# Kernel tuning notes

Hardware: AMD Instinct MI355X
Metric: run time of the kernel (lower is better)

## Reference

```python
import jax, jax.numpy as jnp
import numpy as np

N = 100_000   # nodes
E = 1_600_000 # edges (avg degree 16)
D = 64        # in_channel == out_channel (residual requires equality)
EPS = 1e-5    # BatchNorm1d eps


def setup_inputs() -> dict:
    key = jax.random.key(0)
    ks = jax.random.split(key, 8)
    x = jax.random.normal(ks[0], (N, D), dtype=jnp.float32)
    adj_val = jax.random.uniform(ks[1], (E,), dtype=jnp.float32) * 0.25  # sparse poly_adj values
    W = jax.random.normal(ks[2], (D, D), dtype=jnp.float32) / np.sqrt(D)  # Linear weight [out,in]
    b = jnp.zeros((D,), dtype=jnp.float32)
    gamma = jnp.ones((D,), dtype=jnp.float32)
    beta = jnp.zeros((D,), dtype=jnp.float32)
    adj_row = jax.random.randint(ks[3], (E,), 0, N, dtype=jnp.int32)
    adj_col = jax.random.randint(ks[4], (E,), 0, N, dtype=jnp.int32)
    return {"x": x, "adj_val": adj_val, "W": W, "b": b,
            "gamma": gamma, "beta": beta, "adj_row": adj_row, "adj_col": adj_col}


def reference(x, adj_val, W, b, gamma, beta, adj_row, adj_col):
    # h = poly_adj @ x  (COO SpMM via gather + segment_sum)
    h = jax.ops.segment_sum(adj_val[:, None] * x[adj_col], adj_row, num_segments=N)
    # Linear
    h = h @ W.T + b
    # residual
    h = h + x
    # BatchNorm1d (training-mode batch stats, biased variance)
    mean = jnp.mean(h, axis=0)
    var = jnp.mean(jnp.square(h - mean), axis=0)
    h = (h - mean) * jax.lax.rsqrt(var + EPS) * gamma + beta
    # ReLU (dropout with p=0 is identity)
    h = jax.nn.relu(h)
    return h
```

## Files before the change

### kernel.cpp

```cpp
#include <hip/hip_runtime.h>

#define DCH 64
#define BN_EPS 1e-5f

#define SUPSH 12
#define NSUPMAX 32
#define CAPS 67584
#define CHA 2048
#define CHB 2048
#define CPS 33
#define FPS 128
#define CAPF 704
#define CITER 8
#define SITER 3

__device__ __forceinline__ unsigned bf16pair(float lo, float hi) {
    unsigned ul = (__float_as_uint(lo) + 0x8000u) >> 16;
    unsigned uh = (__float_as_uint(hi) + 0x8000u) & 0xffff0000u;
    return ul | uh;
}
__device__ __forceinline__ float bf_lo(unsigned u) { return __uint_as_float(u << 16); }
__device__ __forceinline__ float bf_hi(unsigned u) { return __uint_as_float(u & 0xffff0000u); }

__global__ __launch_bounds__(256) void gemm_bin(const float* __restrict__ x,
                                                const float* __restrict__ W,
                                                unsigned short* __restrict__ yb,
                                                const int* __restrict__ rows,
                                                const int* __restrict__ cols,
                                                const float* __restrict__ vals,
                                                int* __restrict__ cursA,
                                                int2* __restrict__ edgesA,
                                                int N, int E, int GB, int BB,
                                                int NSUP) {
    __shared__ __align__(16) char smem[51200];
    const int tid = threadIdx.x;
    const int role = blockIdx.x & 1;
    const int idx = blockIdx.x >> 1;

    if (role == 0) {
        if (idx >= GB) return;
        float* xs = (float*)smem;
        float* wt = (float*)(smem + 34816);
        const int blockRow = idx * 128;

#pragma unroll
        for (int jj = 0; jj < 4; ++jj) {
            int idx4 = tid * 16 + jj * 4;
            int o = idx4 >> 6, k = idx4 & 63;
            float4 w4 = *(const float4*)&W[idx4];
            wt[(k + 0) * 64 + o] = w4.x;
            wt[(k + 1) * 64 + o] = w4.y;
            wt[(k + 2) * 64 + o] = w4.z;
            wt[(k + 3) * 64 + o] = w4.w;
        }
#pragma unroll
        for (int jj = 0; jj < 8; ++jj) {
            int f4 = tid + 256 * jj;
            int rl = f4 >> 4, k4 = (f4 & 15) * 4;
            int row = blockRow + rl;
            float4 v = make_float4(0.f, 0.f, 0.f, 0.f);
            if (row < N) v = *(const float4*)&x[row * DCH + k4];
            *(float4*)&xs[rl * 68 + k4] = v;
        }
        __syncthreads();

        const int tc = tid & 7;
        const int tr = tid >> 3;
        const int dc = tc * 8;
        float acc[4][8];
#pragma unroll
        for (int i = 0; i < 4; ++i)
#pragma unroll
            for (int j = 0; j < 8; ++j) acc[i][j] = 0.f;

        for (int k4 = 0; k4 < 16; ++k4) {
            float4 xv[4];
#pragma unroll
            for (int i = 0; i < 4; ++i)
                xv[i] = *(const float4*)&xs[(tr + 32 * i) * 68 + k4 * 4];
#pragma unroll
            for (int kk = 0; kk < 4; ++kk) {
                int k = k4 * 4 + kk;
                float4 w0 = *(const float4*)&wt[k * 64 + dc];
                float4 w1 = *(const float4*)&wt[k * 64 + dc + 4];
#pragma unroll
                for (int i = 0; i < 4; ++i) {
                    float xvi = (kk == 0) ? xv[i].x : (kk == 1) ? xv[i].y
                               : (kk == 2) ? xv[i].z : xv[i].w;
                    acc[i][0] = fmaf(xvi, w0.x, acc[i][0]);
                    acc[i][1] = fmaf(xvi, w0.y, acc[i][1]);
                    acc[i][2] = fmaf(xvi, w0.z, acc[i][2]);
                    acc[i][3] = fmaf(xvi, w0.w, acc[i][3]);
                    acc[i][4] = fmaf(xvi, w1.x, acc[i][4]);
                    acc[i][5] = fmaf(xvi, w1.y, acc[i][5]);
                    acc[i][6] = fmaf(xvi, w1.z, acc[i][6]);
                    acc[i][7] = fmaf(xvi, w1.w, acc[i][7]);
                }
            }
        }
#pragma unroll
        for (int i = 0; i < 4; ++i) {
            int row = blockRow + tr + 32 * i;
            if (row < N) {
                uint4 p;
                p.x = bf16pair(acc[i][0], acc[i][1]);
                p.y = bf16pair(acc[i][2], acc[i][3]);
                p.z = bf16pair(acc[i][4], acc[i][5]);
                p.w = bf16pair(acc[i][6], acc[i][7]);
                *(uint4*)&yb[row * DCH + dc] = p;
            }
        }
    } else {
        if (idx >= BB) return;
        int2* stage = (int2*)smem;
        unsigned char* bOf = (unsigned char*)(smem + 16384);
        int* hist   = (int*)(smem + 18432);
        int* startB = (int*)(smem + 18560);
        int* gbase  = (int*)(smem + 18688);
        const int lane = tid & 63, wave = tid >> 6;
        const int base = idx * CHA;
        const int cnt = min(CHA, E - base);

        for (int i = tid; i < NSUPMAX; i += 256) hist[i] = 0;
        __syncthreads();

        int myr[CITER], mycol[CITER], myrank[CITER];
        float myv[CITER];
#pragma unroll
        for (int it = 0; it < CITER; ++it) {
            int k = tid + it * 256;
            if (k < cnt) {
                int r = rows[base + k];
                myr[it] = r;
                mycol[it] = cols[base + k];
                myv[it] = vals[base + k];
                myrank[it] = atomicAdd(&hist[r >> SUPSH], 1);
            }
        }
        __syncthreads();
        if (wave == 0) {
            int v = (lane < NSUP) ? hist[lane] : 0;
            int inc = v;
#pragma unroll
            for (int off = 1; off < 32; off <<= 1) {
                int u = __shfl_up(inc, off);
                if (lane >= off) inc += u;
            }
            if (lane < NSUP) {
                startB[lane] = inc - v;
                gbase[lane] = v ? atomicAdd(&cursA[lane], v) : 0;
            }
        }
        __syncthreads();
#pragma unroll
        for (int it = 0; it < CITER; ++it) {
            int k = tid + it * 256;
            if (k < cnt) {
                int key = myr[it] >> SUPSH;
                int pos = startB[key] + myrank[it];
                int2 pk;
                pk.x = mycol[it] | ((myr[it] & 4095) << 17);
                pk.y = __float_as_int(myv[it]);
                stage[pos] = pk;
                bOf[pos] = (unsigned char)key;
            }
        }
        __syncthreads();
#pragma unroll
        for (int it = 0; it < CITER; ++it) {
            int i = tid + it * 256;
            if (i < cnt) {
                int s = bOf[i];
                int rel = gbase[s] + (i - startB[s]);
                if (rel < CAPS) edgesA[s * CAPS + rel] = stage[i];
            }
        }
    }
}

__global__ __launch_bounds__(256) void bin_fine(const int2* __restrict__ edgesA,
                                                const int* __restrict__ cursA,
                                                int* __restrict__ cursB,
                                                int2* __restrict__ edgesB) {
    __shared__ int2 stage[CHB];
    __shared__ unsigned char bOf[CHB];
    __shared__ int hist[FPS], startB[FPS], gbase[FPS];
    const int tid = threadIdx.x, lane = tid & 63, wave = tid >> 6;
    const int s = blockIdx.x / CPS;
    const int c = blockIdx.x % CPS;
    const int base = s * CAPS + c * CHB;
    int fill = min(cursA[s], CAPS);
    int cnt = max(0, min(CHB, fill - c * CHB));

    for (int i = tid; i < FPS; i += 256) hist[i] = 0;
    __syncthreads();

    int2 mypk[CITER];
    int myrank[CITER];
#pragma unroll
    for (int it = 0; it < CITER; ++it) {
        int k = tid + it * 256;
        if (k < cnt) {
            int2 p = edgesA[base + k];
            mypk[it] = p;
            myrank[it] = atomicAdd(&hist[(p.x >> 22) & 127], 1);
        }
    }
    __syncthreads();
    if (wave == 0) {
        int v0 = hist[2 * lane], v1 = hist[2 * lane + 1];
        int p = v0 + v1;
        int inc = p;
#pragma unroll
        for (int off = 1; off < 64; off <<= 1) {
            int u = __shfl_up(inc, off);
            if (lane >= off) inc += u;
        }
        int b0 = inc - p;
        startB[2 * lane] = b0;
        startB[2 * lane + 1] = b0 + v0;
        gbase[2 * lane]     = v0 ? atomicAdd(&cursB[s * FPS + 2 * lane], v0) : 0;
        gbase[2 * lane + 1] = v1 ? atomicAdd(&cursB[s * FPS + 2 * lane + 1], v1) : 0;
    }
    __syncthreads();
#pragma unroll
    for (int it = 0; it < CITER; ++it) {
        int k = tid + it * 256;
        if (k < cnt) {
            int2 p = mypk[it];
            int key = (p.x >> 22) & 127;
            int pos = startB[key] + myrank[it];
            stage[pos] = p;
            bOf[pos] = (unsigned char)key;
        }
    }
    __syncthreads();
#pragma unroll
    for (int it = 0; it < CITER; ++it) {
        int i = tid + it * 256;
        if (i < cnt) {
            int f = bOf[i];
            int rel = gbase[f] + (i - startB[f]);
            if (rel < CAPF) edgesB[(size_t)(s * FPS + f) * CAPF + rel] = stage[i];
        }
    }
}

__global__ __launch_bounds__(256) void spmm_sorted(const unsigned short* __restrict__ yb,
                                                   const int* __restrict__ cursB,
                                                   const int2* __restrict__ edges,
                                                   const float* __restrict__ x,
                                                   const float* __restrict__ bias,
                                                   unsigned short* __restrict__ zb,
                                                   float* __restrict__ stats, int N) {
    __shared__ int2 cv[CAPF];
    __shared__ int hist[32];
    __shared__ int startE[33];
    __shared__ float rs[4][64];
    __shared__ float rs2[4][64];

    const int tid = threadIdx.x;
    const int b = blockIdx.x;
    const size_t beg = (size_t)b * CAPF;
    int cnt = min(cursB[b], CAPF);
    const int g = tid >> 3;
    const int q8 = tid & 7;
    const int wave = tid >> 6;
    const int lane = tid & 63;
    const int rowBase = b << 5;

    if (tid < 32) hist[tid] = 0;
    __syncthreads();

    int2 mypk[SITER];
    int myrank[SITER];
#pragma unroll
    for (int it = 0; it < SITER; ++it) {
        int k = tid + it * 256;
        if (k < cnt) {
            int2 p = edges[beg + k];
            mypk[it] = p;
            myrank[it] = atomicAdd(&hist[(p.x >> 17) & 31], 1);
        }
    }
    __syncthreads();
    if (wave == 0) {
        int v = (lane < 32) ? hist[lane] : 0;
        int inc = v;
#pragma unroll
        for (int off = 1; off < 32; off <<= 1) {
            int u = __shfl_up(inc, off);
            if (lane >= off) inc += u;
        }
        if (lane < 32) startE[lane] = inc - v;
        if (lane == 31) startE[32] = inc;
    }
    __syncthreads();
#pragma unroll
    for (int it = 0; it < SITER; ++it) {
        int k = tid + it * 256;
        if (k < cnt) {
            int2 p = mypk[it];
            int key = (p.x >> 17) & 31;
            int2 pc;
            pc.x = p.x & 0x1ffff;
            pc.y = p.y;
            cv[startE[key] + myrank[it]] = pc;
        }
    }
    __syncthreads();

    float bs[8];
    *(float4*)&bs[0] = *(const float4*)&bias[q8 * 8];
    *(float4*)&bs[4] = *(const float4*)&bias[q8 * 8 + 4];

    const int e0 = startE[g];
    const int e1 = startE[g + 1];
    float a[8];
#pragma unroll
    for (int i = 0; i < 8; ++i) a[i] = 0.f;

    for (int j = e0; j < e1; j += 8) {
        int cc[8];
        float vv[8];
#pragma unroll
        for (int u = 0; u < 8; ++u) {
            int idx = j + u;
            bool ok = idx < e1;
            int2 pc = cv[ok ? idx : e0];
            vv[u] = ok ? __int_as_float(pc.y) : 0.f;
            cc[u] = pc.x;
        }
        uint4 yq[8];
#pragma unroll
        for (int u = 0; u < 8; ++u)
            yq[u] = *(const uint4*)&yb[cc[u] * DCH + q8 * 8];
#pragma unroll
        for (int u = 0; u < 8; ++u) {
            a[0] = fmaf(vv[u], bf_lo(yq[u].x), a[0]);
            a[1] = fmaf(vv[u], bf_hi(yq[u].x), a[1]);
            a[2] = fmaf(vv[u], bf_lo(yq[u].y), a[2]);
            a[3] = fmaf(vv[u], bf_hi(yq[u].y), a[3]);
            a[4] = fmaf(vv[u], bf_lo(yq[u].z), a[4]);
            a[5] = fmaf(vv[u], bf_hi(yq[u].z), a[5]);
            a[6] = fmaf(vv[u], bf_lo(yq[u].w), a[6]);
            a[7] = fmaf(vv[u], bf_hi(yq[u].w), a[7]);
        }
    }

    float s[8], s2[8];
#pragma unroll
    for (int i = 0; i < 8; ++i) { s[i] = 0.f; s2[i] = 0.f; }

    {
        int r = rowBase + g;
        if (r < N) {
            float xv[8];
            *(float4*)&xv[0] = *(const float4*)&x[r * DCH + q8 * 8];
            *(float4*)&xv[4] = *(const float4*)&x[r * DCH + q8 * 8 + 4];
            float z[8];
#pragma unroll
            for (int i = 0; i < 8; ++i) {
                z[i] = a[i] + bs[i] + xv[i];
                s[i] += z[i];
                s2[i] = fmaf(z[i], z[i], s2[i]);
            }
            uint4 pz;
            pz.x = bf16pair(z[0], z[1]);
            pz.y = bf16pair(z[2], z[3]);
            pz.z = bf16pair(z[4], z[5]);
            pz.w = bf16pair(z[6], z[7]);
            *(uint4*)&zb[r * DCH + q8 * 8] = pz;
        }
    }

#pragma unroll
    for (int m = 8; m <= 32; m <<= 1) {
#pragma unroll
        for (int i = 0; i < 8; ++i) {
            s[i] += __shfl_xor(s[i], m);
            s2[i] += __shfl_xor(s2[i], m);
        }
    }
    if (lane < 8) {
        *(float4*)&rs[wave][q8 * 8]      = *(float4*)&s[0];
        *(float4*)&rs[wave][q8 * 8 + 4]  = *(float4*)&s[4];
        *(float4*)&rs2[wave][q8 * 8]     = *(float4*)&s2[0];
        *(float4*)&rs2[wave][q8 * 8 + 4] = *(float4*)&s2[4];
    }
    __syncthreads();
    if (tid < 64) {
        float ts  = rs[0][tid] + rs[1][tid] + rs[2][tid] + rs[3][tid];
        float ts2 = rs2[0][tid] + rs2[1][tid] + rs2[2][tid] + rs2[3][tid];
        float* st = stats + ((b & 7) << 7);
        atomicAdd(&st[tid], ts);
        atomicAdd(&st[64 + tid], ts2);
    }
}

__global__ __launch_bounds__(256) void bn_relu(const unsigned short* __restrict__ zb,
                                               float* __restrict__ out,
                                               const float* __restrict__ stats,
                                               const float* __restrict__ gamma,
                                               const float* __restrict__ beta,
                                               int ND8, float invN) {
    __shared__ float lsc[64], lsh[64];
    const int tid = threadIdx.x;
    if (tid < 64) {
        float s = 0.f, s2 = 0.f;
#pragma unroll
        for (int r = 0; r < 8; ++r) {
            s  += stats[r * 128 + tid];
            s2 += stats[r * 128 + 64 + tid];
        }
        float mean = s * invN;
        float var = s2 * invN - mean * mean;
        float sc = gamma[tid] * rsqrtf(var + BN_EPS);
        lsc[tid] = sc;
        lsh[tid] = beta[tid] - mean * sc;
    }
    __syncthreads();

    const int idx0 = blockIdx.x * 256 + tid;
    const int q8 = idx0 & 7;
    float sc[8], sh[8];
#pragma unroll
    for (int i = 0; i < 8; ++i) {
        sc[i] = lsc[q8 * 8 + i];
        sh[i] = lsh[q8 * 8 + i];
    }
    const int stride = gridDim.x * 256;
    for (int i = idx0; i < ND8; i += stride) {
        uint4 zq = *(const uint4*)&zb[i * 8];
        float z[8];
        z[0] = bf_lo(zq.x); z[1] = bf_hi(zq.x);
        z[2] = bf_lo(zq.y); z[3] = bf_hi(zq.y);
        z[4] = bf_lo(zq.z); z[5] = bf_hi(zq.z);
        z[6] = bf_lo(zq.w); z[7] = bf_hi(zq.w);
        float4 o0, o1;
        o0.x = fmaxf(fmaf(z[0], sc[0], sh[0]), 0.f);
        o0.y = fmaxf(fmaf(z[1], sc[1], sh[1]), 0.f);
        o0.z = fmaxf(fmaf(z[2], sc[2], sh[2]), 0.f);
        o0.w = fmaxf(fmaf(z[3], sc[3], sh[3]), 0.f);
        o1.x = fmaxf(fmaf(z[4], sc[4], sh[4]), 0.f);
        o1.y = fmaxf(fmaf(z[5], sc[5], sh[5]), 0.f);
        o1.z = fmaxf(fmaf(z[6], sc[6], sh[6]), 0.f);
        o1.w = fmaxf(fmaf(z[7], sc[7], sh[7]), 0.f);
        *(float4*)&out[i * 8] = o0;
        *(float4*)&out[i * 8 + 4] = o1;
    }
}

extern "C" void kernel_launch(void* const* d_in, const int* in_sizes, int n_in,
                              void* d_out, int out_size, void* d_ws, size_t ws_size,
                              hipStream_t stream) {
    const float* x       = (const float*)d_in[0];
    const float* adj_val = (const float*)d_in[1];
    const float* W       = (const float*)d_in[2];
    const float* b       = (const float*)d_in[3];
    const float* gamma   = (const float*)d_in[4];
    const float* beta    = (const float*)d_in[5];
    const int*   adj_row = (const int*)d_in[6];
    const int*   adj_col = (const int*)d_in[7];
    float* out = (float*)d_out;

    const int N  = in_sizes[0] / DCH;
    const int E  = in_sizes[1];
    const int ND = N * DCH;
    const int NSUP = (N + (1 << SUPSH) - 1) >> SUPSH;
    const int NFB  = NSUP * FPS;

    char* ws = (char*)d_ws;
    float* stats = (float*)ws;
    int* cursA   = (int*)(ws + 4096);
    int* cursB   = (int*)(ws + 4224);
    size_t off = 17024;
    unsigned short* yb = (unsigned short*)(ws + off); off += (size_t)ND * 2;
    off = (off + 127) & ~127ull;
    unsigned short* zb = (unsigned short*)(ws + off); off += (size_t)ND * 2;
    off = (off + 127) & ~127ull;
    int2* edgesA = (int2*)(ws + off);  off += (size_t)NSUP * CAPS * 8;
    int2* edgesB = (int2*)(ws + off);  off += (size_t)NFB * CAPF * 8;

    hipMemsetAsync(ws, 0, 17024, stream);

    const int GB = (N + 127) / 128;
    const int BB = (E + CHA - 1) / CHA;
    const int PAIRS = (GB > BB) ? GB : BB;

    gemm_bin<<<2 * PAIRS, 256, 0, stream>>>(x, W, yb, adj_row, adj_col, adj_val,
                                            cursA, edgesA, N, E, GB, BB, NSUP);
    bin_fine<<<NSUP * CPS, 256, 0, stream>>>(edgesA, cursA, cursB, edgesB);
    spmm_sorted<<<NFB, 256, 0, stream>>>(yb, cursB, edgesB, x, b, zb, stats, N);
    bn_relu<<<1024, 256, 0, stream>>>(zb, out, stats, gamma, beta, ND / 8,
                                      1.0f / (float)N);
}
```

Measured before the change: 176.4 us.

## Co-schedule the dense GEMM with the fine binning pass instead of coarse binning

The dense x·W GEMM blocks move from sharing a launch with the coarse binning pass to sharing one with the fine binning pass. Coarse binning now runs alone as its own kernel. The intent is to balance work across the two launches: the fine pass has a similar block count to the GEMM (about 25*33 against 782), while the coarse pass has about 782 blocks. Kernel count stays the same, so any effect depends on how well the GEMM overlaps with each binning phase.

```diff
diff --git a/kernel.cpp b/kernel.cpp
--- a/kernel.cpp
+++ b/kernel.cpp
@@ -22,16 +22,83 @@
 __device__ __forceinline__ float bf_lo(unsigned u) { return __uint_as_float(u << 16); }
 __device__ __forceinline__ float bf_hi(unsigned u) { return __uint_as_float(u & 0xffff0000u); }
 
-__global__ __launch_bounds__(256) void gemm_bin(const float* __restrict__ x,
-                                                const float* __restrict__ W,
-                                                unsigned short* __restrict__ yb,
-                                                const int* __restrict__ rows,
-                                                const int* __restrict__ cols,
-                                                const float* __restrict__ vals,
-                                                int* __restrict__ cursA,
-                                                int2* __restrict__ edgesA,
-                                                int N, int E, int GB, int BB,
-                                                int NSUP) {
+__global__ __launch_bounds__(256) void bin_coarse(const int* __restrict__ rows,
+                                                  const int* __restrict__ cols,
+                                                  const float* __restrict__ vals,
+                                                  int* __restrict__ cursA,
+                                                  int2* __restrict__ edgesA,
+                                                  int E, int NSUP) {
+    __shared__ int2 stage[CHA];
+    __shared__ unsigned char bOf[CHA];
+    __shared__ int hist[NSUPMAX], startB[NSUPMAX], gbase[NSUPMAX];
+    const int tid = threadIdx.x, lane = tid & 63, wave = tid >> 6;
+    const int base = blockIdx.x * CHA;
+    const int cnt = min(CHA, E - base);
+
+    for (int i = tid; i < NSUPMAX; i += 256) hist[i] = 0;
+    __syncthreads();
+
+    int myr[CITER], mycol[CITER], myrank[CITER];
+    float myv[CITER];
+#pragma unroll
+    for (int it = 0; it < CITER; ++it) {
+        int k = tid + it * 256;
+        if (k < cnt) {
+            int r = rows[base + k];
+            myr[it] = r;
+            mycol[it] = cols[base + k];
+            myv[it] = vals[base + k];
+            myrank[it] = atomicAdd(&hist[r >> SUPSH], 1);
+        }
+    }
+    __syncthreads();
+    if (wave == 0) {
+        int v = (lane < NSUP) ? hist[lane] : 0;
+        int inc = v;
+#pragma unroll
+        for (int off = 1; off < 32; off <<= 1) {
+            int u = __shfl_up(inc, off);
+            if (lane >= off) inc += u;
+        }
+        if (lane < NSUP) {
+            startB[lane] = inc - v;
+            gbase[lane] = v ? atomicAdd(&cursA[lane], v) : 0;
+        }
+    }
+    __syncthreads();
+#pragma unroll
+    for (int it = 0; it < CITER; ++it) {
+        int k = tid + it * 256;
+        if (k < cnt) {
+            int key = myr[it] >> SUPSH;
+            int pos = startB[key] + myrank[it];
+            int2 pk;
+            pk.x = mycol[it] | ((myr[it] & 4095) << 17);
+            pk.y = __float_as_int(myv[it]);
+            stage[pos] = pk;
+            bOf[pos] = (unsigned char)key;
+        }
+    }
+    __syncthreads();
+#pragma unroll
+    for (int it = 0; it < CITER; ++it) {
+        int i = tid + it * 256;
+        if (i < cnt) {
+            int s = bOf[i];
+            int rel = gbase[s] + (i - startB[s]);
+            if (rel < CAPS) edgesA[s * CAPS + rel] = stage[i];
+        }
+    }
+}
+
+__global__ __launch_bounds__(256) void gemm_fine(const float* __restrict__ x,
+                                                 const float* __restrict__ W,
+                                                 unsigned short* __restrict__ yb,
+                                                 const int2* __restrict__ edgesA,
+                                                 const int* __restrict__ cursA,
+                                                 int* __restrict__ cursB,
+                                                 int2* __restrict__ edgesB,
+                                                 int N, int GB, int FB) {
     __shared__ __align__(16) char smem[51200];
     const int tid = threadIdx.x;
     const int role = blockIdx.x & 1;
@@ -111,57 +178,58 @@
             }
         }
     } else {
-        if (idx >= BB) return;
+        if (idx >= FB) return;
         int2* stage = (int2*)smem;
         unsigned char* bOf = (unsigned char*)(smem + 16384);
         int* hist   = (int*)(smem + 18432);
-        int* startB = (int*)(smem + 18560);
-        int* gbase  = (int*)(smem + 18688);
+        int* startB = (int*)(smem + 18944);
+        int* gbase  = (int*)(smem + 19456);
         const int lane = tid & 63, wave = tid >> 6;
-        const int base = idx * CHA;
-        const int cnt = min(CHA, E - base);
-
-        for (int i = tid; i < NSUPMAX; i += 256) hist[i] = 0;
+        const int s = idx / CPS;
+        const int c = idx % CPS;
+        const int base = s * CAPS + c * CHB;
+        int fill = min(cursA[s], CAPS);
+        int cnt = max(0, min(CHB, fill - c * CHB));
+
+        for (int i = tid; i < FPS; i += 256) hist[i] = 0;
         __syncthreads();
 
-        int myr[CITER], mycol[CITER], myrank[CITER];
-        float myv[CITER];
+        int2 mypk[CITER];
+        int myrank[CITER];
 #pragma unroll
         for (int it = 0; it < CITER; ++it) {
             int k = tid + it * 256;
             if (k < cnt) {
-                int r = rows[base + k];
-                myr[it] = r;
-                mycol[it] = cols[base + k];
-                myv[it] = vals[base + k];
-                myrank[it] = atomicAdd(&hist[r >> SUPSH], 1);
+                int2 p = edgesA[base + k];
+                mypk[it] = p;
+                myrank[it] = atomicAdd(&hist[(p.x >> 22) & 127], 1);
             }
         }
         __syncthreads();
         if (wave == 0) {
-            int v = (lane < NSUP) ? hist[lane] : 0;
-            int inc = v;
-#pragma unroll
-            for (int off = 1; off < 32; off <<= 1) {
+            int v0 = hist[2 * lane], v1 = hist[2 * lane + 1];
+            int p = v0 + v1;
+            int inc = p;
+#pragma unroll
+            for (int off = 1; off < 64; off <<= 1) {
                 int u = __shfl_up(inc, off);
                 if (lane >= off) inc += u;
             }
-            if (lane < NSUP) {
-                startB[lane] = inc - v;
-                gbase[lane] = v ? atomicAdd(&cursA[lane], v) : 0;
-            }
+            int b0 = inc - p;
+            startB[2 * lane] = b0;
+            startB[2 * lane + 1] = b0 + v0;
+            gbase[2 * lane]     = v0 ? atomicAdd(&cursB[s * FPS + 2 * lane], v0) : 0;
+            gbase[2 * lane + 1] = v1 ? atomicAdd(&cursB[s * FPS + 2 * lane + 1], v1) : 0;
         }
         __syncthreads();
 #pragma unroll
         for (int it = 0; it < CITER; ++it) {
             int k = tid + it * 256;
             if (k < cnt) {
-                int key = myr[it] >> SUPSH;
+                int2 p = mypk[it];
+                int key = (p.x >> 22) & 127;
                 int pos = startB[key] + myrank[it];
-                int2 pk;
-                pk.x = mycol[it] | ((myr[it] & 4095) << 17);
-                pk.y = __float_as_int(myv[it]);
-                stage[pos] = pk;
+                stage[pos] = p;
                 bOf[pos] = (unsigned char)key;
             }
         }
@@ -170,78 +238,10 @@
         for (int it = 0; it < CITER; ++it) {
             int i = tid + it * 256;
             if (i < cnt) {
-                int s = bOf[i];
-                int rel = gbase[s] + (i - startB[s]);
-                if (rel < CAPS) edgesA[s * CAPS + rel] = stage[i];
-            }
-        }
-    }
-}
-
-__global__ __launch_bounds__(256) void bin_fine(const int2* __restrict__ edgesA,
-                                                const int* __restrict__ cursA,
-                                                int* __restrict__ cursB,
-                                                int2* __restrict__ edgesB) {
-    __shared__ int2 stage[CHB];
-    __shared__ unsigned char bOf[CHB];
-    __shared__ int hist[FPS], startB[FPS], gbase[FPS];
-    const int tid = threadIdx.x, lane = tid & 63, wave = tid >> 6;
-    const int s = blockIdx.x / CPS;
-    const int c = blockIdx.x % CPS;
-    const int base = s * CAPS + c * CHB;
-    int fill = min(cursA[s], CAPS);
-    int cnt = max(0, min(CHB, fill - c * CHB));
-
-    for (int i = tid; i < FPS; i += 256) hist[i] = 0;
-    __syncthreads();
-
-    int2 mypk[CITER];
-    int myrank[CITER];
-#pragma unroll
-    for (int it = 0; it < CITER; ++it) {
-        int k = tid + it * 256;
-        if (k < cnt) {
-            int2 p = edgesA[base + k];
-            mypk[it] = p;
-            myrank[it] = atomicAdd(&hist[(p.x >> 22) & 127], 1);
-        }
-    }
-    __syncthreads();
-    if (wave == 0) {
-        int v0 = hist[2 * lane], v1 = hist[2 * lane + 1];
-        int p = v0 + v1;
-        int inc = p;
-#pragma unroll
-        for (int off = 1; off < 64; off <<= 1) {
-            int u = __shfl_up(inc, off);
-            if (lane >= off) inc += u;
-        }
-        int b0 = inc - p;
-        startB[2 * lane] = b0;
-        startB[2 * lane + 1] = b0 + v0;
-        gbase[2 * lane]     = v0 ? atomicAdd(&cursB[s * FPS + 2 * lane], v0) : 0;
-        gbase[2 * lane + 1] = v1 ? atomicAdd(&cursB[s * FPS + 2 * lane + 1], v1) : 0;
-    }
-    __syncthreads();
-#pragma unroll
-    for (int it = 0; it < CITER; ++it) {
-        int k = tid + it * 256;
-        if (k < cnt) {
-            int2 p = mypk[it];
-            int key = (p.x >> 22) & 127;
-            int pos = startB[key] + myrank[it];
-            stage[pos] = p;
-            bOf[pos] = (unsigned char)key;
-        }
-    }
-    __syncthreads();
-#pragma unroll
-    for (int it = 0; it < CITER; ++it) {
-        int i = tid + it * 256;
-        if (i < cnt) {
-            int f = bOf[i];
-            int rel = gbase[f] + (i - startB[f]);
-            if (rel < CAPF) edgesB[(size_t)(s * FPS + f) * CAPF + rel] = stage[i];
+                int f = bOf[i];
+                int rel = gbase[f] + (i - startB[f]);
+                if (rel < CAPF) edgesB[(size_t)(s * FPS + f) * CAPF + rel] = stage[i];
+            }
         }
     }
 }
@@ -486,11 +486,13 @@
 
     const int GB = (N + 127) / 128;
     const int BB = (E + CHA - 1) / CHA;
-    const int PAIRS = (GB > BB) ? GB : BB;
-
-    gemm_bin<<<2 * PAIRS, 256, 0, stream>>>(x, W, yb, adj_row, adj_col, adj_val,
-                                            cursA, edgesA, N, E, GB, BB, NSUP);
-    bin_fine<<<NSUP * CPS, 256, 0, stream>>>(edgesA, cursA, cursB, edgesB);
+    const int FB = NSUP * CPS;
+    const int PAIRS = (GB > FB) ? GB : FB;
+
+    bin_coarse<<<BB, 256, 0, stream>>>(adj_row, adj_col, adj_val, cursA,
+                                       edgesA, E, NSUP);
+    gemm_fine<<<2 * PAIRS, 256, 0, stream>>>(x, W, yb, edgesA, cursA, cursB,
+                                             edgesB, N, GB, FB);
     spmm_sorted<<<NFB, 256, 0, stream>>>(yb, cursB, edgesB, x, b, zb, stats, N);
     bn_relu<<<1024, 256, 0, stream>>>(zb, out, stats, gamma, beta, ND / 8,
                                       1.0f / (float)N);
```

Measured after the change: 180.0 us. 2.0% more time.

## Replace two-level edge binning with per-row atomic slot buckets

Applied to the files above, without the earlier changes.

Drops the coarse/fine counting-sort kernels and the in-block row sort. Each edge atomically claims a slot in a fixed 64-entry bucket for its row, and the SpMM kernel loads each block's 32 row buckets directly. This removes one kernel launch and two scatter passes. In exchange it adds many global atomics, uncoalesced writes, full-bucket reads that include empty slots, and it drops edges for rows with degree above 64. The bn_relu grid size is also doubled.

```diff
diff --git a/kernel.cpp b/kernel.cpp
--- a/kernel.cpp
+++ b/kernel.cpp
@@ -3,16 +3,9 @@
 #define DCH 64
 #define BN_EPS 1e-5f
 
-#define SUPSH 12
-#define NSUPMAX 32
-#define CAPS 67584
+#define CAPR 64
 #define CHA 2048
-#define CHB 2048
-#define CPS 33
-#define FPS 128
-#define CAPF 704
 #define CITER 8
-#define SITER 3
 
 __device__ __forceinline__ unsigned bf16pair(float lo, float hi) {
     unsigned ul = (__float_as_uint(lo) + 0x8000u) >> 16;
@@ -28,10 +21,9 @@
                                                 const int* __restrict__ rows,
                                                 const int* __restrict__ cols,
                                                 const float* __restrict__ vals,
-                                                int* __restrict__ cursA,
-                                                int2* __restrict__ edgesA,
-                                                int N, int E, int GB, int BB,
-                                                int NSUP) {
+                                                int* __restrict__ cursR,
+                                                int2* __restrict__ edgesR,
+                                                int N, int E, int GB, int BB) {
     __shared__ __align__(16) char smem[51200];
     const int tid = threadIdx.x;
     const int role = blockIdx.x & 1;
@@ -112,210 +104,59 @@
         }
     } else {
         if (idx >= BB) return;
-        int2* stage = (int2*)smem;
-        unsigned char* bOf = (unsigned char*)(smem + 16384);
-        int* hist   = (int*)(smem + 18432);
-        int* startB = (int*)(smem + 18560);
-        int* gbase  = (int*)(smem + 18688);
-        const int lane = tid & 63, wave = tid >> 6;
         const int base = idx * CHA;
         const int cnt = min(CHA, E - base);
-
-        for (int i = tid; i < NSUPMAX; i += 256) hist[i] = 0;
-        __syncthreads();
-
-        int myr[CITER], mycol[CITER], myrank[CITER];
-        float myv[CITER];
 #pragma unroll
         for (int it = 0; it < CITER; ++it) {
             int k = tid + it * 256;
             if (k < cnt) {
                 int r = rows[base + k];
-                myr[it] = r;
-                mycol[it] = cols[base + k];
-                myv[it] = vals[base + k];
-                myrank[it] = atomicAdd(&hist[r >> SUPSH], 1);
+                int c = cols[base + k];
+                float v = vals[base + k];
+                int pos = atomicAdd(&cursR[r], 1);
+                if (pos < CAPR) {
+                    int2 e;
+                    e.x = c;
+                    e.y = __float_as_int(v);
+                    edgesR[((size_t)r << 6) + pos] = e;
+                }
             }
         }
-        __syncthreads();
-        if (wave == 0) {
-            int v = (lane < NSUP) ? hist[lane] : 0;
-            int inc = v;
-#pragma unroll
-            for (int off = 1; off < 32; off <<= 1) {
-                int u = __shfl_up(inc, off);
-                if (lane >= off) inc += u;
-            }
-            if (lane < NSUP) {
-                startB[lane] = inc - v;
-                gbase[lane] = v ? atomicAdd(&cursA[lane], v) : 0;
-            }
-        }
-        __syncthreads();
-#pragma unroll
-        for (int it = 0; it < CITER; ++it) {
-            int k = tid + it * 256;
-            if (k < cnt) {
-                int key = myr[it] >> SUPSH;
-                int pos = startB[key] + myrank[it];
-                int2 pk;
-                pk.x = mycol[it] | ((myr[it] & 4095) << 17);
-                pk.y = __float_as_int(myv[it]);
-                stage[pos] = pk;
-                bOf[pos] = (unsigned char)key;
-            }
-        }
-        __syncthreads();
-#pragma unroll
-        for (int it = 0; it < CITER; ++it) {
-            int i = tid + it * 256;
-            if (i < cnt) {
-                int s = bOf[i];
-                int rel = gbase[s] + (i - startB[s]);
-                if (rel < CAPS) edgesA[s * CAPS + rel] = stage[i];
-            }
-        }
-    }
-}
-
-__global__ __launch_bounds__(256) void bin_fine(const int2* __restrict__ edgesA,
-                                                const int* __restrict__ cursA,
-                                                int* __restrict__ cursB,
-                                                int2* __restrict__ edgesB) {
-    __shared__ int2 stage[CHB];
-    __shared__ unsigned char bOf[CHB];
-    __shared__ int hist[FPS], startB[FPS], gbase[FPS];
-    const int tid = threadIdx.x, lane = tid & 63, wave = tid >> 6;
-    const int s = blockIdx.x / CPS;
-    const int c = blockIdx.x % CPS;
-    const int base = s * CAPS + c * CHB;
-    int fill = min(cursA[s], CAPS);
-    int cnt = max(0, min(CHB, fill - c * CHB));
-
-    for (int i = tid; i < FPS; i += 256) hist[i] = 0;
-    __syncthreads();
-
-    int2 mypk[CITER];
-    int myrank[CITER];
-#pragma unroll
-    for (int it = 0; it < CITER; ++it) {
-        int k = tid + it * 256;
-        if (k < cnt) {
-            int2 p = edgesA[base + k];
-            mypk[it] = p;
-            myrank[it] = atomicAdd(&hist[(p.x >> 22) & 127], 1);
-        }
-    }
-    __syncthreads();
-    if (wave == 0) {
-        int v0 = hist[2 * lane], v1 = hist[2 * lane + 1];
-        int p = v0 + v1;
-        int inc = p;
-#pragma unroll
-        for (int off = 1; off < 64; off <<= 1) {
-            int u = __shfl_up(inc, off);
-            if (lane >= off) inc += u;
-        }
-        int b0 = inc - p;
-        startB[2 * lane] = b0;
-        startB[2 * lane + 1] = b0 + v0;
-        gbase[2 * lane]     = v0 ? atomicAdd(&cursB[s * FPS + 2 * lane], v0) : 0;
-        gbase[2 * lane + 1] = v1 ? atomicAdd(&cursB[s * FPS + 2 * lane + 1], v1) : 0;
-    }
-    __syncthreads();
-#pragma unroll
-    for (int it = 0; it < CITER; ++it) {
-        int k = tid + it * 256;
-        if (k < cnt) {
-            int2 p = mypk[it];
-            int key = (p.x >> 22) & 127;
-            int pos = startB[key] + myrank[it];
-            stage[pos] = p;
-            bOf[pos] = (unsigned char)key;
-        }
-    }
-    __syncthreads();
-#pragma unroll
-    for (int it = 0; it < CITER; ++it) {
-        int i = tid + it * 256;
-        if (i < cnt) {
-            int f = bOf[i];
-            int rel = gbase[f] + (i - startB[f]);
-            if (rel < CAPF) edgesB[(size_t)(s * FPS + f) * CAPF + rel] = stage[i];
-        }
-    }
-}
-
-__global__ __launch_bounds__(256) void spmm_sorted(const unsigned short* __restrict__ yb,
-                                                   const int* __restrict__ cursB,
-                                                   const int2* __restrict__ edges,
+    }
+}
+
+__global__ __launch_bounds__(256) void spmm_direct(const unsigned short* __restrict__ yb,
+                                                   const int* __restrict__ cursR,
+                                                   const int2* __restrict__ edgesR,
                                                    const float* __restrict__ x,
                                                    const float* __restrict__ bias,
                                                    unsigned short* __restrict__ zb,
                                                    float* __restrict__ stats, int N) {
-    __shared__ int2 cv[CAPF];
-    __shared__ int hist[32];
-    __shared__ int startE[33];
+    __shared__ int2 cv[32 * CAPR];
     __shared__ float rs[4][64];
     __shared__ float rs2[4][64];
 
     const int tid = threadIdx.x;
     const int b = blockIdx.x;
-    const size_t beg = (size_t)b * CAPF;
-    int cnt = min(cursB[b], CAPF);
     const int g = tid >> 3;
     const int q8 = tid & 7;
     const int wave = tid >> 6;
     const int lane = tid & 63;
     const int rowBase = b << 5;
-
-    if (tid < 32) hist[tid] = 0;
-    __syncthreads();
-
-    int2 mypk[SITER];
-    int myrank[SITER];
-#pragma unroll
-    for (int it = 0; it < SITER; ++it) {
-        int k = tid + it * 256;
-        if (k < cnt) {
-            int2 p = edges[beg + k];
-            mypk[it] = p;
-            myrank[it] = atomicAdd(&hist[(p.x >> 17) & 31], 1);
-        }
-    }
-    __syncthreads();
-    if (wave == 0) {
-        int v = (lane < 32) ? hist[lane] : 0;
-        int inc = v;
-#pragma unroll
-        for (int off = 1; off < 32; off <<= 1) {
-            int u = __shfl_up(inc, off);
-            if (lane >= off) inc += u;
-        }
-        if (lane < 32) startE[lane] = inc - v;
-        if (lane == 31) startE[32] = inc;
-    }
-    __syncthreads();
-#pragma unroll
-    for (int it = 0; it < SITER; ++it) {
-        int k = tid + it * 256;
-        if (k < cnt) {
-            int2 p = mypk[it];
-            int key = (p.x >> 17) & 31;
-            int2 pc;
-            pc.x = p.x & 0x1ffff;
-            pc.y = p.y;
-            cv[startE[key] + myrank[it]] = pc;
-        }
-    }
+    const int r = rowBase + g;
+
+    const uint4* src = (const uint4*)&edgesR[(size_t)rowBase << 6];
+#pragma unroll
+    for (int i = 0; i < 4; ++i)
+        ((uint4*)cv)[tid + i * 256] = src[tid + i * 256];
     __syncthreads();
 
     float bs[8];
     *(float4*)&bs[0] = *(const float4*)&bias[q8 * 8];
     *(float4*)&bs[4] = *(const float4*)&bias[q8 * 8 + 4];
 
-    const int e0 = startE[g];
-    const int e1 = startE[g + 1];
+    const int e0 = g << 6;
+    const int e1 = e0 + ((r < N) ? min(cursR[r], CAPR) : 0);
     float a[8];
 #pragma unroll
     for (int i = 0; i < 8; ++i) a[i] = 0.f;
@@ -352,26 +193,23 @@
 #pragma unroll
     for (int i = 0; i < 8; ++i) { s[i] = 0.f; s2[i] = 0.f; }
 
-    {
-        int r = rowBase + g;
-        if (r < N) {
-            float xv[8];
-            *(float4*)&xv[0] = *(const float4*)&x[r * DCH + q8 * 8];
-            *(float4*)&xv[4] = *(const float4*)&x[r * DCH + q8 * 8 + 4];
-            float z[8];
-#pragma unroll
-            for (int i = 0; i < 8; ++i) {
-                z[i] = a[i] + bs[i] + xv[i];
-                s[i] += z[i];
-                s2[i] = fmaf(z[i], z[i], s2[i]);
-            }
-            uint4 pz;
-            pz.x = bf16pair(z[0], z[1]);
-            pz.y = bf16pair(z[2], z[3]);
-            pz.z = bf16pair(z[4], z[5]);
-            pz.w = bf16pair(z[6], z[7]);
-            *(uint4*)&zb[r * DCH + q8 * 8] = pz;
-        }
+    if (r < N) {
+        float xv[8];
+        *(float4*)&xv[0] = *(const float4*)&x[r * DCH + q8 * 8];
+        *(float4*)&xv[4] = *(const float4*)&x[r * DCH + q8 * 8 + 4];
+        float z[8];
+#pragma unroll
+        for (int i = 0; i < 8; ++i) {
+            z[i] = a[i] + bs[i] + xv[i];
+            s[i] += z[i];
+            s2[i] = fmaf(z[i], z[i], s2[i]);
+        }
+        uint4 pz;
+        pz.x = bf16pair(z[0], z[1]);
+        pz.y = bf16pair(z[2], z[3]);
+        pz.z = bf16pair(z[4], z[5]);
+        pz.w = bf16pair(z[6], z[7]);
+        *(uint4*)&zb[r * DCH + q8 * 8] = pz;
     }
 
 #pragma unroll
@@ -467,31 +305,28 @@
     const int N  = in_sizes[0] / DCH;
     const int E  = in_sizes[1];
     const int ND = N * DCH;
-    const int NSUP = (N + (1 << SUPSH) - 1) >> SUPSH;
-    const int NFB  = NSUP * FPS;
+    const int NR32 = (N + 31) / 32;
 
     char* ws = (char*)d_ws;
     float* stats = (float*)ws;
-    int* cursA   = (int*)(ws + 4096);
-    int* cursB   = (int*)(ws + 4224);
-    size_t off = 17024;
+    int* cursR   = (int*)(ws + 4096);
+    size_t curs_bytes = (size_t)NR32 * 32 * 4;
+    size_t off = (4096 + curs_bytes + 127) & ~127ull;
     unsigned short* yb = (unsigned short*)(ws + off); off += (size_t)ND * 2;
     off = (off + 127) & ~127ull;
     unsigned short* zb = (unsigned short*)(ws + off); off += (size_t)ND * 2;
     off = (off + 127) & ~127ull;
-    int2* edgesA = (int2*)(ws + off);  off += (size_t)NSUP * CAPS * 8;
-    int2* edgesB = (int2*)(ws + off);  off += (size_t)NFB * CAPF * 8;
-
-    hipMemsetAsync(ws, 0, 17024, stream);
+    int2* edgesR = (int2*)(ws + off);  off += (size_t)NR32 * 32 * CAPR * 8;
+
+    hipMemsetAsync(ws, 0, 4096 + curs_bytes, stream);
 
     const int GB = (N + 127) / 128;
     const int BB = (E + CHA - 1) / CHA;
     const int PAIRS = (GB > BB) ? GB : BB;
 
     gemm_bin<<<2 * PAIRS, 256, 0, stream>>>(x, W, yb, adj_row, adj_col, adj_val,
-                                            cursA, edgesA, N, E, GB, BB, NSUP);
-    bin_fine<<<NSUP * CPS, 256, 0, stream>>>(edgesA, cursA, cursB, edgesB);
-    spmm_sorted<<<NFB, 256, 0, stream>>>(yb, cursB, edgesB, x, b, zb, stats, N);
-    bn_relu<<<1024, 256, 0, stream>>>(zb, out, stats, gamma, beta, ND / 8,
+                                            cursR, edgesR, N, E, GB, BB);
+    spmm_direct<<<NR32, 256, 0, stream>>>(yb, cursR, edgesR, x, b, zb, stats, N);
+    bn_relu<<<2048, 256, 0, stream>>>(zb, out, stats, gamma, beta, ND / 8,
                                       1.0f / (float)N);
 }
```

New measurement: 239.9 us. 1.36x slower.
